# Kernel tuning notes

Measured on AMD Instinct MI355X. Metric: run time of the kernel, lower is better.

## Reference

```python
import jax, jax.numpy as jnp
import numpy as np
import math

B, S, D, H, L, D_OUT = 8, 1024, 1024, 16, 2, 1024
DK = D // H
LN_EPS = 1e-8


def _ln(x, g, b):
    m = jnp.mean(x, axis=-1, keepdims=True)
    var = jnp.mean((x - m) ** 2, axis=-1, keepdims=True)
    return (x - m) / jnp.sqrt(var + LN_EPS) * g + b


def setup_inputs() -> dict:
    key = jax.random.key(0)
    ks = jax.random.split(key, 16)
    s = 0.02
    return {
        "q": jax.random.normal(ks[0], (B, S, D), jnp.float32),
        "k": jax.random.normal(ks[1], (B, S, D), jnp.float32),
        "v": jax.random.normal(ks[2], (B, S, D), jnp.float32),
        "attn_mask": jnp.ones((B, S, S), jnp.int32),
        # per-layer stacked params
        "Wqkv": jax.random.normal(ks[3], (L, 3, D, D), jnp.float32) * s,  # [out,in]
        "bqkv": jnp.zeros((L, 3, D), jnp.float32),
        "Wo": jax.random.normal(ks[4], (L, D, D), jnp.float32) * s,
        "bo": jnp.zeros((L, D), jnp.float32),
        "ln1_g": jnp.ones((L, D), jnp.float32),
        "ln1_b": jnp.zeros((L, D), jnp.float32),
        "ln2_g": jnp.ones((L, D), jnp.float32),
        "ln2_b": jnp.zeros((L, D), jnp.float32),
        "Wc1": jax.random.normal(ks[5], (L, D, D), jnp.float32) * s,  # conv1d k=1 == linear
        "bc1": jnp.zeros((L, D), jnp.float32),
        "Wc2": jax.random.normal(ks[6], (L, D, D), jnp.float32) * s,
        "bc2": jnp.zeros((L, D), jnp.float32),
        "last_g": jnp.ones((D,), jnp.float32),
        "last_b": jnp.zeros((D,), jnp.float32),
        "Wfc": jax.random.normal(ks[7], (D_OUT, D), jnp.float32) * s,
        "bfc": jnp.zeros((D_OUT,), jnp.float32),
    }


def reference(q, k, v, attn_mask, Wqkv, bqkv, Wo, bo, ln1_g, ln1_b, ln2_g, ln2_b,
              Wc1, bc1, Wc2, bc2, last_g, last_b, Wfc, bfc):
    scale = 1.0 / math.sqrt(DK)
    mask = (attn_mask == 0)[:, None, :, :]  # [B,1,S,S] broadcast over heads

    def proj(x, W, b):
        # linear [out,in] then split heads -> [B,H,S,dk]
        y = jnp.einsum('bsd,od->bso', x, W) + b
        return y.reshape(B, S, H, DK).transpose(0, 2, 1, 3)

    for i in range(L):
        Q = _ln(q, ln1_g[i], ln1_b[i])
        qh = proj(Q, Wqkv[i, 0], bqkv[i, 0])
        kh = proj(k, Wqkv[i, 1], bqkv[i, 1])
        vh = proj(v, Wqkv[i, 2], bqkv[i, 2])
        scores = jnp.einsum('bhqd,bhkd->bhqk', qh, kh) * scale
        scores = jnp.clip(scores, -30.0, 30.0)
        scores = jnp.where(mask, -1e9, scores) + 1e-5
        p = jax.nn.softmax(scores, axis=-1)
        x = jnp.einsum('bhqk,bhkd->bhqd', p, vh)
        x = x.transpose(0, 2, 1, 3).reshape(B, S, D)
        x = jax.nn.relu(jnp.einsum('bsd,od->bso', x, Wo[i]) + bo[i])
        k = k + x
        k = _ln(k, ln2_g[i], ln2_b[i])
        # PointWiseFeedForward: conv2(conv1(x)) + x, kernel_size=1, no activation
        h = jnp.einsum('bsd,od->bso', k, Wc1[i]) + bc1[i]
        h = jnp.einsum('bsd,od->bso', h, Wc2[i]) + bc2[i]
        k = k + h
        q = k
        v = k
    out = _ln(k, last_g, last_b)
    return jnp.einsum('bsd,od->bso', out, Wfc) + bfc
```

## Files before the change

### kernel.cpp

```cpp
#include <hip/hip_runtime.h>

typedef __attribute__((ext_vector_type(8))) short s8x;
typedef __attribute__((ext_vector_type(4))) float f4x;
typedef unsigned short u16;
typedef unsigned int u32;

#define DEV static __device__ __forceinline__

DEV u16 f2b(float f) {
    union { float f; u32 u; } v; v.f = f;
    u32 r = v.u + 0x7FFFu + ((v.u >> 16) & 1u);
    return (u16)(r >> 16);
}

DEV float b2f(u16 x) {
    union { u32 u; float f; } v; v.u = (u32)x << 16;
    return v.f;
}

DEV u32 pk2(float lo, float hi) {
    u32 r;
    asm("v_cvt_pk_bf16_f32 %0, %1, %2" : "=v"(r) : "v"(lo), "v"(hi));
    return r;
}

DEV float exp2_raw(float x) {
    float r;
    asm("v_exp_f32 %0, %1" : "=v"(r) : "v"(x));
    return r;
}

DEV void gload16(const void* g, void* lds) {
    __builtin_amdgcn_global_load_lds(
        (const __attribute__((address_space(1))) void*)g,
        (__attribute__((address_space(3))) void*)lds, 16, 0, 0);
}

#define GK 1024
#define BM 128
#define BN 128
#define BK 64


DEV void stage_unit(const u16* __restrict__ g, char* l, int tid) {
#pragma unroll
    for (int i = 0; i < 2; ++i) {
        int db = i * 8192 + tid * 16;
        int row = db >> 7;
        int cs = ((db >> 4) & 7) ^ (row & 7);
        gload16(g + (size_t)row * 1024 + cs * 8, l + db);
    }
}

DEV s8x lds_frag(const char* Lbase, int row, int kk, int lg) {
    int cb = (kk * 64 + lg * 16) ^ ((row & 7) << 4);
    return *(const s8x*)(Lbase + row * 128 + cb);
}

template<int FLAGS, int NN>
__global__ __launch_bounds__(512, 2) void gemm8(
    const u16* __restrict__ A, const u16* __restrict__ W,
    const float* __restrict__ bias, const u16* __restrict__ res,
    float* __restrict__ outf, u16* __restrict__ outb, float scl)
{
    constexpr bool RELU = (FLAGS & 1) != 0;
    constexpr bool RES  = (FLAGS & 2) != 0;
    constexpr bool WF   = (FLAGS & 4) != 0;
    constexpr bool WB   = (FLAGS & 8) != 0;
    constexpr bool RBIA = (FLAGS & 16) != 0;

    __shared__ __attribute__((aligned(16))) u16 As[3][256 * 64];
    __shared__ __attribute__((aligned(16))) u16 Bs[3][128 * 64];

    const int tid = threadIdx.x, lane = tid & 63, wid = tid >> 6;
    const int l15 = lane & 15, lg = lane >> 4;
    const int wm = wid >> 1, wn = wid & 1;
    const int bm = blockIdx.x, bn = blockIdx.y;

    const u16* Ab = A + (size_t)bm * 256 * GK;
    const u16* Wb = W + (size_t)bn * 128 * GK;

    f4x acc[4][4];
#pragma unroll
    for (int i = 0; i < 4; ++i)
#pragma unroll
        for (int j = 0; j < 4; ++j) { f4x z = {0.f, 0.f, 0.f, 0.f}; acc[i][j] = z; }

    char* a0 = (char*)As[0]; char* a1 = (char*)As[1]; char* a2 = (char*)As[2];
    char* b0 = (char*)Bs[0]; char* b1 = (char*)Bs[1]; char* b2 = (char*)Bs[2];

    stage_unit(Ab + 0 * 64,                 a0,        tid);
    stage_unit(Ab + 128 * GK + 0 * 64,      a0 + 16384, tid);
    stage_unit(Wb + 0 * 64,                 b0,        tid);
    stage_unit(Ab + 1 * 64,                 a1,        tid);
    stage_unit(Ab + 128 * GK + 1 * 64,      a1 + 16384, tid);
    stage_unit(Wb + 1 * 64,                 b1,        tid);
    asm volatile("s_waitcnt vmcnt(6)" ::: "memory");
    __builtin_amdgcn_s_barrier();

    for (int t = 0; t < 16; ++t) {
        const bool st = (t < 14);
        s8x bfr[4][2], afr[2][2];
#pragma unroll
        for (int ni = 0; ni < 4; ++ni)
#pragma unroll
            for (int kk = 0; kk < 2; ++kk)
                bfr[ni][kk] = lds_frag(b0, wn * 64 + ni * 16 + l15, kk, lg);
#pragma unroll
        for (int mi = 0; mi < 2; ++mi)
#pragma unroll
            for (int kk = 0; kk < 2; ++kk)
                afr[mi][kk] = lds_frag(a0, wm * 64 + mi * 16 + l15, kk, lg);
        if (st) {
            stage_unit(Ab + (t + 2) * 64,            a2,         tid);
            stage_unit(Ab + 128 * GK + (t + 2) * 64, a2 + 16384, tid);
        }
        __builtin_amdgcn_s_barrier();
        asm volatile("s_waitcnt lgkmcnt(0)" ::: "memory");
        __builtin_amdgcn_sched_barrier(0);
        __builtin_amdgcn_s_setprio(1);
#pragma unroll
        for (int kk = 0; kk < 2; ++kk)
#pragma unroll
            for (int mi = 0; mi < 2; ++mi)
#pragma unroll
                for (int ni = 0; ni < 4; ++ni)
                    acc[mi][ni] = __builtin_amdgcn_mfma_f32_16x16x32_bf16(afr[mi][kk], bfr[ni][kk], acc[mi][ni], 0, 0, 0);
        __builtin_amdgcn_s_setprio(0);
        __builtin_amdgcn_s_barrier();

        s8x afr2[2][2];
#pragma unroll
        for (int mi = 0; mi < 2; ++mi)
#pragma unroll
            for (int kk = 0; kk < 2; ++kk)
                afr2[mi][kk] = lds_frag(a0, wm * 64 + (mi + 2) * 16 + l15, kk, lg);
        if (st) stage_unit(Wb + (t + 2) * 64, b2, tid);
        __builtin_amdgcn_s_barrier();
        asm volatile("s_waitcnt lgkmcnt(0)" ::: "memory");
        __builtin_amdgcn_sched_barrier(0);
        __builtin_amdgcn_s_setprio(1);
#pragma unroll
        for (int kk = 0; kk < 2; ++kk)
#pragma unroll
            for (int mi = 0; mi < 2; ++mi)
#pragma unroll
                for (int ni = 0; ni < 4; ++ni)
                    acc[mi + 2][ni] = __builtin_amdgcn_mfma_f32_16x16x32_bf16(afr2[mi][kk], bfr[ni][kk], acc[mi + 2][ni], 0, 0, 0);
        __builtin_amdgcn_s_setprio(0);
        if (st) asm volatile("s_waitcnt vmcnt(6)" ::: "memory");
        else    asm volatile("s_waitcnt vmcnt(0)" ::: "memory");
        __builtin_amdgcn_s_barrier();

        char* tA = a0; a0 = a1; a1 = a2; a2 = tA;
        char* tB = b0; b0 = b1; b1 = b2; b2 = tB;
    }

#pragma unroll
    for (int ni = 0; ni < 4; ++ni) {
        int gcol = bn * 128 + wn * 64 + ni * 16 + l15;
        float bvc = RBIA ? 0.f : bias[gcol];
#pragma unroll
        for (int mi = 0; mi < 4; ++mi) {
            int grow0 = bm * 256 + wm * 64 + mi * 16 + lg * 4;
#pragma unroll
            for (int r = 0; r < 4; ++r) {
                float bv = RBIA ? bias[grow0 + r] : bvc;
                float v = (acc[mi][ni][r] + bv) * scl;
                if (RELU) v = fmaxf(v, 0.f);
                size_t oidx = (size_t)(grow0 + r) * NN + gcol;
                if (RES) v += b2f(res[oidx]);
                if (WF) outf[oidx] = v;
                if (WB) outb[oidx] = f2b(v);
            }
        }
    }
}

__global__ __launch_bounds__(256) void gemm_z2(
    const u16* __restrict__ A0, const u16* __restrict__ W0, const float* __restrict__ b0,
    u16* __restrict__ o0, float s0,
    const u16* __restrict__ A1, const u16* __restrict__ W1, const float* __restrict__ b1,
    u16* __restrict__ o1, float s1)
{
    const int z = blockIdx.z;
    const u16* A = z ? A1 : A0;
    const u16* W = z ? W1 : W0;
    const float* bias = z ? b1 : b0;
    u16* outb = z ? o1 : o0;
    const float scl = z ? s1 : s0;

    __shared__ __attribute__((aligned(16))) u16 As[2][BM * BK];
    __shared__ __attribute__((aligned(16))) u16 Bs[2][BN * BK];

    const int tid  = threadIdx.x;
    const int lane = tid & 63;
    const int wid  = tid >> 6;
    const int wr = wid >> 1, wc = wid & 1;
    const int bm = blockIdx.x, bn = blockIdx.y;
    const int l15 = lane & 15;
    const int lg  = lane >> 4;

    const u16* Ab = A + (size_t)bm * BM * GK;
    const u16* Wb = W + (size_t)bn * BN * GK;

    const int prow = tid >> 3;
    const int pcol = (tid & 7) * 8;

    f4x acc[4][4];
#pragma unroll
    for (int i = 0; i < 4; ++i)
#pragma unroll
        for (int j = 0; j < 4; ++j) { f4x z_ = {0.f, 0.f, 0.f, 0.f}; acc[i][j] = z_; }

#pragma unroll
    for (int c = 0; c < 4; ++c) {
        int row = c * 32 + prow;
        gload16(Ab + (size_t)row * GK + pcol, &As[0][row * BK + pcol]);
    }
#pragma unroll
    for (int c = 0; c < 4; ++c) {
        int row = c * 32 + prow;
        gload16(Wb + (size_t)row * GK + pcol, &Bs[0][row * BK + pcol]);
    }

    const int nkt = GK / BK;
    int cur = 0;
    for (int kt = 0; kt < nkt; ++kt) {
        __syncthreads();
        if (kt + 1 < nkt) {
            const u16* Ak = Ab + (kt + 1) * BK;
            const u16* Wk = Wb + (kt + 1) * BK;
#pragma unroll
            for (int c = 0; c < 4; ++c) {
                int row = c * 32 + prow;
                gload16(Ak + (size_t)row * GK + pcol, &As[cur ^ 1][row * BK + pcol]);
            }
#pragma unroll
            for (int c = 0; c < 4; ++c) {
                int row = c * 32 + prow;
                gload16(Wk + (size_t)row * GK + pcol, &Bs[cur ^ 1][row * BK + pcol]);
            }
        }
        const u16* Ac = As[cur];
        const u16* Bc = Bs[cur];
#pragma unroll
        for (int kk = 0; kk < 2; ++kk) {
            s8x a[4], b[4];
#pragma unroll
            for (int mi = 0; mi < 4; ++mi)
                a[mi] = *(const s8x*)(Ac + (wr * 64 + mi * 16 + l15) * BK + kk * 32 + lg * 8);
#pragma unroll
            for (int ni = 0; ni < 4; ++ni)
                b[ni] = *(const s8x*)(Bc + (wc * 64 + ni * 16 + l15) * BK + kk * 32 + lg * 8);
#pragma unroll
            for (int mi = 0; mi < 4; ++mi)
#pragma unroll
                for (int ni = 0; ni < 4; ++ni)
                    acc[mi][ni] = __builtin_amdgcn_mfma_f32_16x16x32_bf16(a[mi], b[ni], acc[mi][ni], 0, 0, 0);
        }
        cur ^= 1;
    }

#pragma unroll
    for (int ni = 0; ni < 4; ++ni) {
        int gcol = bn * BN + wc * 64 + ni * 16 + l15;
        float bvc = bias[gcol];
#pragma unroll
        for (int mi = 0; mi < 4; ++mi) {
            int grow0 = bm * BM + wr * 64 + mi * 16 + lg * 4;
#pragma unroll
            for (int r = 0; r < 4; ++r) {
                float v = (acc[mi][ni][r] + bvc) * scl;
                outb[(size_t)(grow0 + r) * 1024 + gcol] = f2b(v);
            }
        }
    }
}

__global__ __launch_bounds__(512) void attn_kernel(
    const u16* __restrict__ Qm, const u16* __restrict__ Km, const u16* __restrict__ Vt,
    const u32* __restrict__ maskw, const u32* __restrict__ rowfl,
    u16* __restrict__ Om)
{
    const int bh = blockIdx.x;
    const int b  = bh >> 4;
    const int h  = bh & 15;
    const int qt = blockIdx.y;
    const int tid = threadIdx.x, lane = tid & 63, wid = tid >> 6;
    const int l15 = lane & 15, lg = lane >> 4;

    __shared__ __attribute__((aligned(16))) u16 Ks[2][64 * 64];
    __shared__ __attribute__((aligned(16))) u16 Vs[2][64 * 64];
    __shared__ __attribute__((aligned(16))) u16 Ps[8][16][64];
    __shared__ int anymask;

    const size_t rowbase = (size_t)b * 1024;
    const int hoff = h * 64;

    if (tid == 0) anymask = 0;

    const int so   = tid * 16;
    const int srow = so >> 7;
    const int sch  = ((so >> 4) & 7) ^ (srow & 7);
    const int vswz = (l15 & 7) << 4;

    const u16* Kbase = Km + rowbase * 1024 + hoff;
    const u16* Vbase = Vt + (size_t)(hoff + srow) * 8192 + b * 1024;

    gload16(Kbase + (size_t)srow * 1024 + sch * 8, (char*)Ks[0] + so);
    gload16(Vbase + sch * 8,                       (char*)Vs[0] + so);

    __syncthreads();
    if (tid < 128) {
        if (rowfl[rowbase + qt * 128 + tid]) atomicOr(&anymask, 1);
    }

    const int qrow = qt * 128 + wid * 16 + l15;
    s8x qf[2];
#pragma unroll
    for (int kk = 0; kk < 2; ++kk)
        qf[kk] = *(const s8x*)(Qm + (rowbase + qrow) * 1024 + hoff + kk * 32 + lg * 8);

    f4x o[4];
#pragma unroll
    for (int d = 0; d < 4; ++d) { f4x z = {0.f, 0.f, 0.f, 0.f}; o[d] = z; }
    float lrun = 0.f;

    __syncthreads();
    const int am = anymask;
    const float CLIP = 43.2808512f;

    int cur = 0;
    for (int kt = 0; kt < 16; ++kt) {
        if (kt < 15) {
            gload16(Kbase + (size_t)(kt + 1) * 64 * 1024 + (size_t)srow * 1024 + sch * 8,
                    (char*)Ks[cur ^ 1] + so);
            gload16(Vbase + (kt + 1) * 64 + sch * 8, (char*)Vs[cur ^ 1] + so);
        }

        f4x sc[4];
#pragma unroll
        for (int ni = 0; ni < 4; ++ni) { f4x z = {0.f, 0.f, 0.f, 0.f}; sc[ni] = z; }
        __builtin_amdgcn_s_setprio(1);
#pragma unroll
        for (int kk = 0; kk < 2; ++kk) {
#pragma unroll
            for (int ni = 0; ni < 4; ++ni) {
                int row = ni * 16 + l15;
                int cb  = (kk * 64 + lg * 16) ^ ((row & 7) << 4);
                s8x kf = *(const s8x*)((const char*)Ks[cur] + row * 128 + cb);
                sc[ni] = __builtin_amdgcn_mfma_f32_16x16x32_bf16(kf, qf[kk], sc[ni], 0, 0, 0);
            }
        }
        __builtin_amdgcn_s_setprio(0);

        if (am) {
            int qg = qt * 128 + wid * 16 + l15;
#pragma unroll
            for (int ni = 0; ni < 4; ++ni)
#pragma unroll
                for (int r = 0; r < 4; ++r) {
                    int kcol = kt * 64 + ni * 16 + lg * 4 + r;
                    u32 wb_ = maskw[(rowbase + qg) * 32 + (kcol >> 5)];
                    if (wb_ & (1u << (kcol & 31))) sc[ni][r] = -1e9f;
                }
        }

        float s = 0.f;
#pragma unroll
        for (int ni = 0; ni < 4; ++ni)
#pragma unroll
            for (int r = 0; r < 4; ++r) {
                float p = exp2_raw(fminf(sc[ni][r], CLIP));
                sc[ni][r] = p;
                s += p;
            }
        s += __shfl_xor(s, 16);
        s += __shfl_xor(s, 32);
        lrun += s;

#pragma unroll
        for (int ni = 0; ni < 4; ++ni) {
            uint2 w; w.x = pk2(sc[ni][0], sc[ni][1]); w.y = pk2(sc[ni][2], sc[ni][3]);
            *(uint2*)((char*)&Ps[wid][l15][0] + ((ni * 32 + lg * 8) ^ vswz)) = w;
        }
        s8x pa[2];
#pragma unroll
        for (int kk = 0; kk < 2; ++kk)
            pa[kk] = *(const s8x*)((const char*)&Ps[wid][l15][0] + ((kk * 64 + lg * 16) ^ vswz));

        __builtin_amdgcn_s_setprio(1);
#pragma unroll
        for (int dt = 0; dt < 4; ++dt)
#pragma unroll
            for (int kk = 0; kk < 2; ++kk) {
                int row = dt * 16 + l15;
                int cb  = (kk * 64 + lg * 16) ^ ((row & 7) << 4);
                s8x vf = *(const s8x*)((const char*)Vs[cur] + row * 128 + cb);
                o[dt] = __builtin_amdgcn_mfma_f32_16x16x32_bf16(pa[kk], vf, o[dt], 0, 0, 0);
            }
        __builtin_amdgcn_s_setprio(0);

        __syncthreads();
        cur ^= 1;
    }

    float rl = 1.f / lrun;
    float rlr[4];
#pragma unroll
    for (int r = 0; r < 4; ++r) rlr[r] = __shfl(rl, lg * 4 + r);
#pragma unroll
    for (int dt = 0; dt < 4; ++dt) {
        int gc = hoff + dt * 16 + l15;
#pragma unroll
        for (int r = 0; r < 4; ++r) {
            int gr = qt * 128 + wid * 16 + lg * 4 + r;
            Om[(rowbase + gr) * 1024 + gc] = f2b(o[dt][r] * rlr[r]);
        }
    }
}

__global__ __launch_bounds__(256) void ln_f(
    const float* __restrict__ x, const float* __restrict__ g, const float* __restrict__ bb,
    u16* __restrict__ yb)
{
    const int wid = threadIdx.x >> 6, lane = threadIdx.x & 63;
    const size_t row = (size_t)blockIdx.x * 4 + wid;
    const float* xr = x + row * 1024;
    float4 v[4];
    float s = 0.f, s2 = 0.f;
#pragma unroll
    for (int c = 0; c < 4; ++c) {
        v[c] = *(const float4*)(xr + c * 256 + lane * 4);
        s  += v[c].x + v[c].y + v[c].z + v[c].w;
        s2 += v[c].x * v[c].x + v[c].y * v[c].y + v[c].z * v[c].z + v[c].w * v[c].w;
    }
#pragma unroll
    for (int m = 32; m >= 1; m >>= 1) { s += __shfl_xor(s, m); s2 += __shfl_xor(s2, m); }
    float mean = s * (1.f / 1024.f);
    float var  = s2 * (1.f / 1024.f) - mean * mean;
    float rs = rsqrtf(var + 1e-8f);
#pragma unroll
    for (int c = 0; c < 4; ++c) {
        int col = c * 256 + lane * 4;
        float4 gv = *(const float4*)(g + col);
        float4 bv = *(const float4*)(bb + col);
        ushort4 o4 = make_ushort4(
            f2b((v[c].x - mean) * rs * gv.x + bv.x),
            f2b((v[c].y - mean) * rs * gv.y + bv.y),
            f2b((v[c].z - mean) * rs * gv.z + bv.z),
            f2b((v[c].w - mean) * rs * gv.w + bv.w));
        *(ushort4*)(yb + row * 1024 + col) = o4;
    }
}

__global__ __launch_bounds__(256) void ln_b(
    const u16* __restrict__ x, const float* __restrict__ g, const float* __restrict__ bb,
    u16* __restrict__ yb)
{
    const int wid = threadIdx.x >> 6, lane = threadIdx.x & 63;
    const size_t row = (size_t)blockIdx.x * 4 + wid;
    const u16* xr = x + row * 1024 + lane * 16;
    s8x v0 = *(const s8x*)xr;
    s8x v1 = *(const s8x*)(xr + 8);
    float f[16];
    float s = 0.f, s2 = 0.f;
#pragma unroll
    for (int j = 0; j < 8; ++j) { f[j] = b2f((u16)v0[j]); f[8 + j] = b2f((u16)v1[j]); }
#pragma unroll
    for (int j = 0; j < 16; ++j) { s += f[j]; s2 += f[j] * f[j]; }
#pragma unroll
    for (int m = 32; m >= 1; m >>= 1) { s += __shfl_xor(s, m); s2 += __shfl_xor(s2, m); }
    float mean = s * (1.f / 1024.f);
    float var  = s2 * (1.f / 1024.f) - mean * mean;
    float rs = rsqrtf(var + 1e-8f);
    const int col0 = lane * 16;
    u16 ov[16];
#pragma unroll
    for (int c = 0; c < 4; ++c) {
        float4 gv = *(const float4*)(g + col0 + c * 4);
        float4 bv = *(const float4*)(bb + col0 + c * 4);
        ov[c * 4 + 0] = f2b((f[c * 4 + 0] - mean) * rs * gv.x + bv.x);
        ov[c * 4 + 1] = f2b((f[c * 4 + 1] - mean) * rs * gv.y + bv.y);
        ov[c * 4 + 2] = f2b((f[c * 4 + 2] - mean) * rs * gv.z + bv.z);
        ov[c * 4 + 3] = f2b((f[c * 4 + 3] - mean) * rs * gv.w + bv.w);
    }
    u16* yr = yb + row * 1024 + col0;
    *(ushort4*)(yr + 0)  = make_ushort4(ov[0], ov[1], ov[2], ov[3]);
    *(ushort4*)(yr + 4)  = make_ushort4(ov[4], ov[5], ov[6], ov[7]);
    *(ushort4*)(yr + 8)  = make_ushort4(ov[8], ov[9], ov[10], ov[11]);
    *(ushort4*)(yr + 12) = make_ushort4(ov[12], ov[13], ov[14], ov[15]);
}

__global__ __launch_bounds__(256) void cvt_kernel(const float* __restrict__ x, u16* __restrict__ y, int n4)
{
    int i = blockIdx.x * 256 + threadIdx.x;
    if (i < n4) {
        float4 v = *(const float4*)(x + (size_t)i * 4);
        ushort4 o = make_ushort4(f2b(v.x), f2b(v.y), f2b(v.z), f2b(v.w));
        *(ushort4*)(y + (size_t)i * 4) = o;
    }
}

__global__ __launch_bounds__(256) void cvtT_kernel(const float* __restrict__ X, u16* __restrict__ Y)
{
    __shared__ u16 T[64][65];
    const int l = blockIdx.z;
    const int j0 = blockIdx.y * 64;
    const int i0 = blockIdx.x * 64;
    const float* Xl = X + (size_t)l * 1024 * 1024;
    u16* Yl = Y + (size_t)l * 1024 * 1024;
    const int tr = threadIdx.x >> 4;
    const int tc = threadIdx.x & 15;
#pragma unroll
    for (int k = 0; k < 4; ++k) {
        int j = tr + k * 16;
        float4 v = *(const float4*)(Xl + (size_t)(j0 + j) * 1024 + i0 + tc * 4);
        T[tc * 4 + 0][j] = f2b(v.x);
        T[tc * 4 + 1][j] = f2b(v.y);
        T[tc * 4 + 2][j] = f2b(v.z);
        T[tc * 4 + 3][j] = f2b(v.w);
    }
    __syncthreads();
    const int wr_ = threadIdx.x >> 3;
    const int wc_ = threadIdx.x & 7;
#pragma unroll
    for (int k = 0; k < 2; ++k) {
        int i = wr_ + k * 32;
        u16 tmp[8];
#pragma unroll
        for (int e = 0; e < 8; ++e) tmp[e] = T[i][wc_ * 8 + e];
        *(ushort4*)(Yl + (size_t)(i0 + i) * 1024 + j0 + wc_ * 8)     = make_ushort4(tmp[0], tmp[1], tmp[2], tmp[3]);
        *(ushort4*)(Yl + (size_t)(i0 + i) * 1024 + j0 + wc_ * 8 + 4) = make_ushort4(tmp[4], tmp[5], tmp[6], tmp[7]);
    }
}

__global__ __launch_bounds__(256) void matvec_kernel(const float* __restrict__ W2, const float* __restrict__ b1,
                                                     const float* __restrict__ b2, float* __restrict__ outv)
{
    const int wid = threadIdx.x >> 6, lane = threadIdx.x & 63;
    int row = blockIdx.x * 4 + wid;
    int l = row >> 10, o = row & 1023;
    const float* wr_ = W2 + (size_t)l * 1024 * 1024 + (size_t)o * 1024;
    const float* b1l = b1 + l * 1024;
    float s = 0.f;
#pragma unroll
    for (int c = 0; c < 4; ++c) {
        float4 w = *(const float4*)(wr_ + c * 256 + lane * 4);
        float4 bv = *(const float4*)(b1l + c * 256 + lane * 4);
        s += w.x * bv.x + w.y * bv.y + w.z * bv.z + w.w * bv.w;
    }
#pragma unroll
    for (int m = 32; m >= 1; m >>= 1) s += __shfl_xor(s, m);
    if (lane == 0) outv[row] = s + b2[l * 1024 + o];
}

__global__ __launch_bounds__(256) void mask_kernel(const int* __restrict__ am, u32* __restrict__ mw)
{
    size_t idx = (size_t)blockIdx.x * 256 + threadIdx.x;
    unsigned long long bal = __ballot(am[idx] == 0);
    int lane = threadIdx.x & 63;
    if (lane == 0)  mw[idx >> 5] = (u32)bal;
    if (lane == 32) mw[idx >> 5] = (u32)(bal >> 32);
}

__global__ __launch_bounds__(256) void rowflag_kernel(const u32* __restrict__ mw, u32* __restrict__ rf)
{
    int r = blockIdx.x * 256 + threadIdx.x;
    u32 o = 0;
#pragma unroll
    for (int i = 0; i < 32; ++i) o |= mw[r * 32 + i];
    rf[r] = o;
}

extern "C" void kernel_launch(void* const* d_in, const int* in_sizes, int n_in,
                              void* d_out, int out_size, void* d_ws, size_t ws_size,
                              hipStream_t stream)
{
    (void)in_sizes; (void)n_in; (void)out_size; (void)ws_size;

    const float* q_in  = (const float*)d_in[0];
    const float* k_in  = (const float*)d_in[1];
    const float* v_in  = (const float*)d_in[2];
    const int*   amask = (const int*)d_in[3];
    const float* Wqkv  = (const float*)d_in[4];
    const float* bqkv  = (const float*)d_in[5];
    const float* Wo    = (const float*)d_in[6];
    const float* bo    = (const float*)d_in[7];
    const float* ln1g  = (const float*)d_in[8];
    const float* ln1b  = (const float*)d_in[9];
    const float* ln2g  = (const float*)d_in[10];
    const float* ln2b  = (const float*)d_in[11];
    const float* Wc1   = (const float*)d_in[12];
    const float* bc1   = (const float*)d_in[13];
    const float* Wc2   = (const float*)d_in[14];
    const float* bc2   = (const float*)d_in[15];
    const float* lastg = (const float*)d_in[16];
    const float* lastb = (const float*)d_in[17];
    const float* Wfc   = (const float*)d_in[18];
    const float* bfc   = (const float*)d_in[19];
    float* out = (float*)d_out;

    char* base = (char*)d_ws;
    size_t off = 0;
    auto alloc = [&](size_t bytes) -> char* {
        char* p = base + off;
        off = (off + bytes + 255) & ~(size_t)255;
        return p;
    };
    const size_t M1 = 1024 * 1024;
    const size_t MT = 8192 * 1024;
    u16* wqkv_b = (u16*)alloc(6 * M1 * 2);
    u16* wo_b   = (u16*)alloc(2 * M1 * 2);
    u16* wcomb  = (u16*)alloc(2 * M1 * 2);
    u16* wfc_b  = (u16*)alloc(M1 * 2);
    float* bcomb = (float*)alloc(2 * 1024 * 4);
    float* zb    = (float*)alloc(1024 * 4);
    u32* maskw  = (u32*)alloc(8192 * 32 * 4);
    u32* rowfl  = (u32*)alloc(8192 * 4);
    u16* t0 = (u16*)alloc(MT * 2);
    u16* t1 = (u16*)alloc(MT * 2);
    u16* qh = (u16*)alloc(MT * 2);
    u16* kh = (u16*)alloc(MT * 2);
    u16* vt = (u16*)alloc(MT * 2);
    u16* xb = (u16*)alloc(MT * 2);
    u16* x2 = (u16*)alloc(MT * 2);
    u16* wc1t  = qh;
    u16* wc2_b = kh;

    cvt_kernel<<<6 * M1 / 1024, 256, 0, stream>>>(Wqkv, wqkv_b, (int)(6 * M1 / 4));
    cvt_kernel<<<2 * M1 / 1024, 256, 0, stream>>>(Wo,   wo_b,   (int)(2 * M1 / 4));
    cvt_kernel<<<M1 / 1024, 256, 0, stream>>>(Wfc, wfc_b, (int)(M1 / 4));
    cvt_kernel<<<2 * M1 / 1024, 256, 0, stream>>>(Wc2, wc2_b, (int)(2 * M1 / 4));
    cvtT_kernel<<<dim3(16, 16, 2), 256, 0, stream>>>(Wc1, wc1t);
    hipMemsetAsync(zb, 0, 1024 * 4, stream);
    gemm_z2<<<dim3(8, 8, 2), 256, 0, stream>>>(
        wc2_b, wc1t, zb, wcomb, 1.f,
        wc2_b + M1, wc1t + M1, zb, wcomb + M1, 1.f);
    matvec_kernel<<<512, 256, 0, stream>>>(Wc2, bc1, bc2, bcomb);
    mask_kernel<<<32768, 256, 0, stream>>>(amask, maskw);
    rowflag_kernel<<<32, 256, 0, stream>>>(maskw, rowfl);

    dim3 g8(8192 / 256, 1024 / 128);
    dim3 v8(1024 / 256, 8192 / 128);
    const float QS = 0.125f * 1.44269504f;
    const int D = 1024;
    for (int i = 0; i < 2; ++i) {
        if (i == 0) {
            ln_f<<<2048, 256, 0, stream>>>(q_in, ln1g, ln1b, t0);
            cvt_kernel<<<8192, 256, 0, stream>>>(k_in, x2, (int)(MT / 4));
            cvt_kernel<<<8192, 256, 0, stream>>>(v_in, xb, (int)(MT / 4));
        } else {
            ln_b<<<2048, 256, 0, stream>>>(x2, ln1g + i * D, ln1b + i * D, t0);
        }
        gemm8<8, 1024><<<g8, 512, 0, stream>>>(t0, wqkv_b + (size_t)(i * 3 + 0) * M1,
                                               bqkv + (i * 3 + 0) * D, nullptr, nullptr, qh, QS);
        gemm8<8, 1024><<<g8, 512, 0, stream>>>(x2, wqkv_b + (size_t)(i * 3 + 1) * M1,
                                               bqkv + (i * 3 + 1) * D, nullptr, nullptr, kh, 1.f);
        const u16* vin_b = (i == 0) ? xb : x2;
        gemm8<8 | 16, 8192><<<v8, 512, 0, stream>>>(wqkv_b + (size_t)(i * 3 + 2) * M1, vin_b,
                                                    bqkv + (i * 3 + 2) * D, nullptr, nullptr, vt, 1.f);
        attn_kernel<<<dim3(128, 8), 512, 0, stream>>>(qh, kh, vt, maskw, rowfl, t0);
        gemm8<1 | 2 | 8, 1024><<<g8, 512, 0, stream>>>(t0, wo_b + (size_t)i * M1,
                                                       bo + i * D, x2, nullptr, t1, 1.f);
        ln_b<<<2048, 256, 0, stream>>>(t1, ln2g + i * D, ln2b + i * D, xb);
        gemm8<2 | 8, 1024><<<g8, 512, 0, stream>>>(xb, wcomb + (size_t)i * M1,
                                                   bcomb + i * 1024, xb, nullptr, x2, 1.f);
    }
    ln_b<<<2048, 256, 0, stream>>>(x2, lastg, lastb, t0);
    gemm8<4, 1024><<<g8, 512, 0, stream>>>(t0, wfc_b, bfc, nullptr, out, nullptr, 1.f);
}
```

Before: 509.2 us.

## Triple-buffer K/V tiles in attention with explicit vmcnt waits

Moves the attention kernel's K/V shared-memory staging from double to triple buffering, prefetching two tiles ahead and rotating buffer pointers. The full __syncthreads at the end of each iteration becomes a partial s_waitcnt vmcnt plus a raw s_barrier, so only the next tile's loads must land before moving on. The Q fragment load is also hoisted before the first barrier. This is meant to hide global-load latency, at the cost of 16KB more LDS per block, which may reduce occupancy.

Result: no change. 504.6 us (-0.9%).

```diff
diff --git a/kernel.cpp b/kernel.cpp
--- a/kernel.cpp
+++ b/kernel.cpp
@@ -290,8 +290,8 @@
     const int tid = threadIdx.x, lane = tid & 63, wid = tid >> 6;
     const int l15 = lane & 15, lg = lane >> 4;
 
-    __shared__ __attribute__((aligned(16))) u16 Ks[2][64 * 64];
-    __shared__ __attribute__((aligned(16))) u16 Vs[2][64 * 64];
+    __shared__ __attribute__((aligned(16))) u16 Ks[3][64 * 64];
+    __shared__ __attribute__((aligned(16))) u16 Vs[3][64 * 64];
     __shared__ __attribute__((aligned(16))) u16 Ps[8][16][64];
     __shared__ int anymask;
 
@@ -305,38 +305,42 @@
     const int sch  = ((so >> 4) & 7) ^ (srow & 7);
     const int vswz = (l15 & 7) << 4;
 
-    const u16* Kbase = Km + rowbase * 1024 + hoff;
-    const u16* Vbase = Vt + (size_t)(hoff + srow) * 8192 + b * 1024;
-
-    gload16(Kbase + (size_t)srow * 1024 + sch * 8, (char*)Ks[0] + so);
-    gload16(Vbase + sch * 8,                       (char*)Vs[0] + so);
+    const u16* Kbase = Km + rowbase * 1024 + hoff + (size_t)srow * 1024 + sch * 8;
+    const u16* Vbase = Vt + (size_t)(hoff + srow) * 8192 + b * 1024 + sch * 8;
+
+    char* kc0 = (char*)Ks[0]; char* kc1 = (char*)Ks[1]; char* kc2 = (char*)Ks[2];
+    char* vc0 = (char*)Vs[0]; char* vc1 = (char*)Vs[1]; char* vc2 = (char*)Vs[2];
+
+    gload16(Kbase + 0 * 64 * 1024, kc0 + so);
+    gload16(Vbase + 0 * 64,        vc0 + so);
+    gload16(Kbase + 1 * 64 * 1024, kc1 + so);
+    gload16(Vbase + 1 * 64,        vc1 + so);
+
+    const int qrow = qt * 128 + wid * 16 + l15;
+    s8x qf[2];
+#pragma unroll
+    for (int kk = 0; kk < 2; ++kk)
+        qf[kk] = *(const s8x*)(Qm + (rowbase + qrow) * 1024 + hoff + kk * 32 + lg * 8);
 
     __syncthreads();
     if (tid < 128) {
         if (rowfl[rowbase + qt * 128 + tid]) atomicOr(&anymask, 1);
     }
 
-    const int qrow = qt * 128 + wid * 16 + l15;
-    s8x qf[2];
-#pragma unroll
-    for (int kk = 0; kk < 2; ++kk)
-        qf[kk] = *(const s8x*)(Qm + (rowbase + qrow) * 1024 + hoff + kk * 32 + lg * 8);
-
     f4x o[4];
 #pragma unroll
     for (int d = 0; d < 4; ++d) { f4x z = {0.f, 0.f, 0.f, 0.f}; o[d] = z; }
     float lrun = 0.f;
 
+    asm volatile("s_waitcnt vmcnt(0)" ::: "memory");
     __syncthreads();
     const int am = anymask;
     const float CLIP = 43.2808512f;
 
-    int cur = 0;
     for (int kt = 0; kt < 16; ++kt) {
-        if (kt < 15) {
-            gload16(Kbase + (size_t)(kt + 1) * 64 * 1024 + (size_t)srow * 1024 + sch * 8,
-                    (char*)Ks[cur ^ 1] + so);
-            gload16(Vbase + (kt + 1) * 64 + sch * 8, (char*)Vs[cur ^ 1] + so);
+        if (kt + 2 < 16) {
+            gload16(Kbase + (size_t)(kt + 2) * 64 * 1024, kc2 + so);
+            gload16(Vbase + (kt + 2) * 64,                vc2 + so);
         }
 
         f4x sc[4];
@@ -349,7 +353,7 @@
             for (int ni = 0; ni < 4; ++ni) {
                 int row = ni * 16 + l15;
                 int cb  = (kk * 64 + lg * 16) ^ ((row & 7) << 4);
-                s8x kf = *(const s8x*)((const char*)Ks[cur] + row * 128 + cb);
+                s8x kf = *(const s8x*)(kc0 + row * 128 + cb);
                 sc[ni] = __builtin_amdgcn_mfma_f32_16x16x32_bf16(kf, qf[kk], sc[ni], 0, 0, 0);
             }
         }
@@ -397,13 +401,17 @@
             for (int kk = 0; kk < 2; ++kk) {
                 int row = dt * 16 + l15;
                 int cb  = (kk * 64 + lg * 16) ^ ((row & 7) << 4);
-                s8x vf = *(const s8x*)((const char*)Vs[cur] + row * 128 + cb);
+                s8x vf = *(const s8x*)(vc0 + row * 128 + cb);
                 o[dt] = __builtin_amdgcn_mfma_f32_16x16x32_bf16(pa[kk], vf, o[dt], 0, 0, 0);
             }
         __builtin_amdgcn_s_setprio(0);
 
-        __syncthreads();
-        cur ^= 1;
+        if (kt + 2 < 16)      asm volatile("s_waitcnt vmcnt(2)" ::: "memory");
+        else if (kt + 1 < 16) asm volatile("s_waitcnt vmcnt(0)" ::: "memory");
+        __builtin_amdgcn_s_barrier();
+
+        char* tk = kc0; kc0 = kc1; kc1 = kc2; kc2 = tk;
+        char* tv = vc0; vc0 = vc1; vc1 = vc2; vc2 = tv;
     }
 
     float rl = 1.f / lrun;
```
